# Optimization experiments

Measured on AMD Instinct MI355X. Metric: run time of the kernel, lower is better.

## Reference

```python
import jax, jax.numpy as jnp
import numpy as np


def setup_inputs() -> dict:
    key = jax.random.key(0)
    k1, k2, k3 = jax.random.split(key, 3)
    T, B, C, H, W = 8, 4, 128, 96, 96
    h = w = 384  # original visibility-map resolution
    values = jax.random.normal(k1, (T + 1, B, C, H, W), jnp.float32)
    tvmap = jax.random.uniform(k2, (B, 1, h, w), jnp.float32)
    rvmaps = jax.random.uniform(k3, (T, B, 1, h, w), jnp.float32)
    return {"values": values, "tvmap": tvmap, "rvmaps": rvmaps}


def _resize_bin(m, H, W):
    # bilinear resize (half-pixel centers == torch align_corners=False), then > 0.5 threshold
    r = jax.image.resize(m, m.shape[:-2] + (H, W), method="bilinear")
    return (r > 0.5).astype(m.dtype)


def reference(values, tvmap, rvmaps):
    t_feat = values[0]          # [B,C,H,W]
    r_feats = values[1:]        # [T,B,C,H,W]
    T, B, C, H, W = r_feats.shape

    tv = _resize_bin(tvmap, H, W)                           # [B,1,H,W]
    rv = jax.vmap(lambda m: _resize_bin(m, H, W))(rvmaps)   # [T,B,1,H,W]
    vmap_ = tv[None] * rv                                   # [T,B,1,H,W]

    # per-frame masked similarity score gs
    gs = jnp.sum(vmap_ * t_feat[None] * r_feats, axis=(-1, -2, -3))  # [T,B]
    v_sum = jnp.sum(vmap_[:, :, 0], axis=(-1, -2))                   # [T,B]
    empty = v_sum < 1e-4
    gs = jnp.where(empty, 0.0, gs) / (v_sum + empty.astype(gs.dtype)) / C

    gss = gs.transpose(1, 0)[:, None, :, None, None]   # [B,1,T,1,1]
    vmaps = rv.transpose(1, 2, 0, 3, 4)                # [B,1,T,H,W]

    # masked softmax over frame axis (dim=2) with zero-guard
    mv = gss * vmaps
    mx = jnp.max(mv, axis=2, keepdims=True)
    me = jnp.exp(mv - mx) * vmaps
    ms = jnp.sum(me, axis=2, keepdims=True)
    ms = ms + (ms < 1e-4).astype(ms.dtype)
    c_match = jax.lax.stop_gradient(me / ms)           # [B,1,T,H,W]

    rf = r_feats.transpose(1, 2, 0, 3, 4)              # [B,C,T,H,W]
    c_out = jnp.sum(rf * c_match, axis=2)              # [B,C,H,W]

    c_mask = jnp.sum(c_match * vmaps, axis=2)          # [B,1,H,W]
    c_mask = jax.lax.stop_gradient(1.0 - jnp.mean(c_mask, axis=1, keepdims=True))

    out = jnp.concatenate([t_feat, c_out, c_mask], axis=1)  # [B, 2C+1, H, W]
    return out, c_mask, gs
```

## Files before the change

kernel.cpp:

```cpp
#include <hip/hip_runtime.h>
#include <math.h>

#define T_ 8
#define B_ 4
#define C_ 128
#define HW_ 9216
#define IN_HW_ 147456

__device__ __forceinline__ double resize_px(const float* __restrict__ img, int y, int x) {
  static const double wm[8]  = {0.03125, 0.09375, 0.15625, 0.21875,
                                0.21875, 0.15625, 0.09375, 0.03125};
  static const double w0[8]  = {0.0, 0.0, 0.625/3.5, 0.875/3.5,
                                0.875/3.5, 0.625/3.5, 0.375/3.5, 0.125/3.5};
  static const double w95[8] = {0.125/3.5, 0.375/3.5, 0.625/3.5, 0.875/3.5,
                                0.875/3.5, 0.625/3.5, 0.0, 0.0};
  const double* wy = (y == 0) ? w0 : (y == 95 ? w95 : wm);
  const double* wx = (x == 0) ? w0 : (x == 95 ? w95 : wm);
  double acc = 0.0;
#pragma unroll
  for (int ky = 0; ky < 8; ++ky) {
    double wyv = wy[ky];
    if (wyv == 0.0) continue;
    int jy = 4 * y - 2 + ky;
    const float* row = img + jy * 384;
    double ra = 0.0;
#pragma unroll
    for (int kx = 0; kx < 8; ++kx) {
      double wxv = wx[kx];
      if (wxv == 0.0) continue;
      int jx = 4 * x - 2 + kx;
      ra += wxv * (double)row[jx];
    }
    acc += wyv * ra;
  }
  return acc;
}

__device__ __forceinline__ float block_reduce_sum_256(float v) {
  __shared__ float s[256];
  s[threadIdx.x] = v;
  __syncthreads();
  for (int k = 128; k > 0; k >>= 1) {
    if (threadIdx.x < (unsigned)k) s[threadIdx.x] += s[threadIdx.x + k];
    __syncthreads();
  }
  return s[0];
}

__global__ void k_init(float* __restrict__ v_sum) {
  if (threadIdx.x < T_ * B_) v_sum[threadIdx.x] = 0.f;
}

__global__ void k_tv(const float* __restrict__ tvmap, float* __restrict__ tv) {
  int b = blockIdx.y;
  int p = blockIdx.x * 256 + threadIdx.x;
  const float* img = tvmap + (size_t)b * IN_HW_;
  int y = p / 96, x = p % 96;
  tv[(size_t)b * HW_ + p] = (resize_px(img, y, x) > 0.5) ? 1.0f : 0.0f;
}

__global__ void k_rv(const float* __restrict__ rvmaps, const float* __restrict__ tv,
                     float* __restrict__ rv, float* __restrict__ vm,
                     float* __restrict__ v_sum) {
  int tb = blockIdx.y;
  int b = tb % B_;
  int p = blockIdx.x * 256 + threadIdx.x;
  const float* img = rvmaps + (size_t)tb * IN_HW_;
  int y = p / 96, x = p % 96;
  float rvv = (resize_px(img, y, x) > 0.5) ? 1.0f : 0.0f;
  float vmv = rvv * tv[(size_t)b * HW_ + p];
  rv[(size_t)tb * HW_ + p] = rvv;
  vm[(size_t)tb * HW_ + p] = vmv;
  float s = block_reduce_sum_256(vmv);
  if (threadIdx.x == 0) atomicAdd(&v_sum[tb], s);
}

__global__ __launch_bounds__(256) void k_gs(const float* __restrict__ values,
                                            const float* __restrict__ vm,
                                            float* __restrict__ gs_part) {
  int blk = blockIdx.x;
  int c  = blk % C_;
  int tb = blk / C_;
  int b  = tb % B_;
  const float4* rf  = (const float4*)(values + ((size_t)(B_ + tb) * C_ + c) * HW_);
  const float4* tf  = (const float4*)(values + ((size_t)b * C_ + c) * HW_);
  const float4* vmp = (const float4*)(vm + (size_t)tb * HW_);
  float acc = 0.f;
  for (int i = threadIdx.x; i < HW_ / 4; i += 256) {
    float4 m = vmp[i];
    float4 a = tf[i];
    float4 r = rf[i];
    acc += m.x * a.x * r.x + m.y * a.y * r.y + m.z * a.z * r.z + m.w * a.w * r.w;
  }
  float s = block_reduce_sum_256(acc);
  if (threadIdx.x == 0) gs_part[blk] = s;
}

__global__ void k_gsfin(const float* __restrict__ gs_part, const float* __restrict__ v_sum,
                        float* __restrict__ gs, float* __restrict__ out_gs) {
  int i = threadIdx.x;
  if (i < T_ * B_) {
    float s = 0.f;
    for (int c = 0; c < C_; ++c) s += gs_part[i * C_ + c];
    float vs = v_sum[i];
    bool empty = vs < 1e-4f;
    float g = (empty ? 0.f : s) / (vs + (empty ? 1.f : 0.f)) / (float)C_;
    gs[i] = g;
    out_gs[i] = g;
  }
}

__global__ __launch_bounds__(256) void k_epi(const float* __restrict__ values,
                                             const float* __restrict__ rv,
                                             const float* __restrict__ gs,
                                             float* __restrict__ out,
                                             float* __restrict__ out_cmask) {
  int ctile = blockIdx.x;
  int ptile = blockIdx.y;
  int b     = blockIdx.z;
  __shared__ float gsh[T_];
  if (threadIdx.x < T_) gsh[threadIdx.x] = gs[threadIdx.x * B_ + b];
  __syncthreads();

  int p0 = ptile * 1024 + threadIdx.x * 4;

  float4 rv4[T_];
#pragma unroll
  for (int t = 0; t < T_; ++t)
    rv4[t] = *(const float4*)(rv + ((size_t)(t * B_ + b)) * HW_ + p0);

  float cm[T_][4];
  float cmask[4];
#pragma unroll
  for (int j = 0; j < 4; ++j) {
    float mv[T_];
    float mx = -1e30f;
#pragma unroll
    for (int t = 0; t < T_; ++t) {
      float rvv = ((const float*)&rv4[t])[j];
      mv[t] = gsh[t] * rvv;
      mx = fmaxf(mx, mv[t]);
    }
    float e[T_];
    float ms = 0.f;
#pragma unroll
    for (int t = 0; t < T_; ++t) {
      float rvv = ((const float*)&rv4[t])[j];
      e[t] = expf(mv[t] - mx) * rvv;
      ms += e[t];
    }
    if (ms < 1e-4f) ms += 1.f;
    float inv = 1.f / ms;
    float cs = 0.f;
#pragma unroll
    for (int t = 0; t < T_; ++t) {
      cm[t][j] = e[t] * inv;
      cs += cm[t][j] * ((const float*)&rv4[t])[j];
    }
    cmask[j] = 1.f - cs;
  }

  size_t outb = (size_t)b * 257 * HW_;
#pragma unroll 1
  for (int cc = 0; cc < 8; ++cc) {
    int c = ctile * 8 + cc;
    float4 tf = *(const float4*)(values + ((size_t)b * C_ + c) * HW_ + p0);
    *(float4*)(out + outb + (size_t)c * HW_ + p0) = tf;
    float4 acc = {0.f, 0.f, 0.f, 0.f};
#pragma unroll
    for (int t = 0; t < T_; ++t) {
      const float4 r = *(const float4*)(values +
          ((size_t)((1 + t) * B_ + b) * C_ + c) * HW_ + p0);
      acc.x += cm[t][0] * r.x;
      acc.y += cm[t][1] * r.y;
      acc.z += cm[t][2] * r.z;
      acc.w += cm[t][3] * r.w;
    }
    *(float4*)(out + outb + (size_t)(C_ + c) * HW_ + p0) = acc;
  }
  if (ctile == 0) {
    float4 cmv = {cmask[0], cmask[1], cmask[2], cmask[3]};
    *(float4*)(out + outb + (size_t)256 * HW_ + p0) = cmv;
    *(float4*)(out_cmask + (size_t)b * HW_ + p0) = cmv;
  }
}

extern "C" void kernel_launch(void* const* d_in, const int* in_sizes, int n_in,
                              void* d_out, int out_size, void* d_ws, size_t ws_size,
                              hipStream_t stream) {
  const float* values = (const float*)d_in[0];
  const float* tvmap  = (const float*)d_in[1];
  const float* rvmaps = (const float*)d_in[2];
  float* out = (float*)d_out;

  float* ws      = (float*)d_ws;
  float* tv      = ws;
  float* rv      = tv + (size_t)B_ * HW_;
  float* vm      = rv + (size_t)T_ * B_ * HW_;
  float* gs_part = vm + (size_t)T_ * B_ * HW_;
  float* v_sum   = gs_part + T_ * B_ * C_;
  float* gsar    = v_sum + T_ * B_;

  float* out_cmask = out + (size_t)B_ * 257 * HW_;
  float* out_gs    = out_cmask + (size_t)B_ * HW_;

  hipLaunchKernelGGL(k_init,  dim3(1),                dim3(64),  0, stream, v_sum);
  hipLaunchKernelGGL(k_tv,    dim3(HW_ / 256, B_),    dim3(256), 0, stream, tvmap, tv);
  hipLaunchKernelGGL(k_rv,    dim3(HW_ / 256, T_ * B_), dim3(256), 0, stream, rvmaps, tv, rv, vm, v_sum);
  hipLaunchKernelGGL(k_gs,    dim3(T_ * B_ * C_),     dim3(256), 0, stream, values, vm, gs_part);
  hipLaunchKernelGGL(k_gsfin, dim3(1),                dim3(64),  0, stream, gs_part, v_sum, gsar, out_gs);
  hipLaunchKernelGGL(k_epi,   dim3(16, 9, B_),        dim3(256), 0, stream, values, rv, gsar, out, out_cmask);
}
```

Baseline: 346.0 us.

## Fuse mask kernels, restructure gs reduction, halve epilogue tile, nontemporal stores

```diff
diff --git a/kernel.cpp b/kernel.cpp
--- a/kernel.cpp
+++ b/kernel.cpp
@@ -6,6 +6,9 @@
 #define C_ 128
 #define HW_ 9216
 #define IN_HW_ 147456
+#define NCHUNK 3
+
+typedef float nfloat4 __attribute__((ext_vector_type(4)));
 
 __device__ __forceinline__ double resize_px(const float* __restrict__ img, int y, int x) {
   static const double wm[8]  = {0.03125, 0.09375, 0.15625, 0.21875,
@@ -28,81 +31,86 @@
     for (int kx = 0; kx < 8; ++kx) {
       double wxv = wx[kx];
       if (wxv == 0.0) continue;
-      int jx = 4 * x - 2 + kx;
-      ra += wxv * (double)row[jx];
+      ra += wxv * (double)row[4 * x - 2 + kx];
     }
     acc += wyv * ra;
   }
   return acc;
 }
 
-__device__ __forceinline__ float block_reduce_sum_256(float v) {
+__global__ __launch_bounds__(256) void k_masks(const float* __restrict__ tvmap,
+                                               const float* __restrict__ rvmaps,
+                                               float* __restrict__ rv,
+                                               float* __restrict__ vm,
+                                               float* __restrict__ v_part) {
+  int tb = blockIdx.y;
+  int b = tb % B_;
+  int p = blockIdx.x * 256 + threadIdx.x;
+  int y = p / 96, x = p % 96;
+  float tvv = (resize_px(tvmap + (size_t)b * IN_HW_, y, x) > 0.5) ? 1.0f : 0.0f;
+  float rvv = (resize_px(rvmaps + (size_t)tb * IN_HW_, y, x) > 0.5) ? 1.0f : 0.0f;
+  float vmv = rvv * tvv;
+  rv[(size_t)tb * HW_ + p] = rvv;
+  vm[(size_t)tb * HW_ + p] = vmv;
   __shared__ float s[256];
-  s[threadIdx.x] = v;
+  s[threadIdx.x] = vmv;
   __syncthreads();
   for (int k = 128; k > 0; k >>= 1) {
     if (threadIdx.x < (unsigned)k) s[threadIdx.x] += s[threadIdx.x + k];
     __syncthreads();
   }
-  return s[0];
-}
-
-__global__ void k_init(float* __restrict__ v_sum) {
-  if (threadIdx.x < T_ * B_) v_sum[threadIdx.x] = 0.f;
-}
-
-__global__ void k_tv(const float* __restrict__ tvmap, float* __restrict__ tv) {
-  int b = blockIdx.y;
-  int p = blockIdx.x * 256 + threadIdx.x;
-  const float* img = tvmap + (size_t)b * IN_HW_;
-  int y = p / 96, x = p % 96;
-  tv[(size_t)b * HW_ + p] = (resize_px(img, y, x) > 0.5) ? 1.0f : 0.0f;
-}
-
-__global__ void k_rv(const float* __restrict__ rvmaps, const float* __restrict__ tv,
-                     float* __restrict__ rv, float* __restrict__ vm,
-                     float* __restrict__ v_sum) {
-  int tb = blockIdx.y;
-  int b = tb % B_;
-  int p = blockIdx.x * 256 + threadIdx.x;
-  const float* img = rvmaps + (size_t)tb * IN_HW_;
-  int y = p / 96, x = p % 96;
-  float rvv = (resize_px(img, y, x) > 0.5) ? 1.0f : 0.0f;
-  float vmv = rvv * tv[(size_t)b * HW_ + p];
-  rv[(size_t)tb * HW_ + p] = rvv;
-  vm[(size_t)tb * HW_ + p] = vmv;
-  float s = block_reduce_sum_256(vmv);
-  if (threadIdx.x == 0) atomicAdd(&v_sum[tb], s);
+  if (threadIdx.x == 0) v_part[tb * (HW_ / 256) + blockIdx.x] = s[0];
 }
 
 __global__ __launch_bounds__(256) void k_gs(const float* __restrict__ values,
                                             const float* __restrict__ vm,
                                             float* __restrict__ gs_part) {
-  int blk = blockIdx.x;
-  int c  = blk % C_;
-  int tb = blk / C_;
-  int b  = tb % B_;
-  const float4* rf  = (const float4*)(values + ((size_t)(B_ + tb) * C_ + c) * HW_);
-  const float4* tf  = (const float4*)(values + ((size_t)b * C_ + c) * HW_);
-  const float4* vmp = (const float4*)(vm + (size_t)tb * HW_);
-  float acc = 0.f;
-  for (int i = threadIdx.x; i < HW_ / 4; i += 256) {
-    float4 m = vmp[i];
+  int c     = blockIdx.x;
+  int chunk = blockIdx.y;
+  int b     = blockIdx.z;
+  const float4* tf = (const float4*)(values + ((size_t)b * C_ + c) * HW_);
+  float acc[T_];
+#pragma unroll
+  for (int t = 0; t < T_; ++t) acc[t] = 0.f;
+  int i0 = chunk * (HW_ / 4 / NCHUNK);
+#pragma unroll 1
+  for (int k = 0; k < HW_ / 4 / NCHUNK / 256; ++k) {
+    int i = i0 + k * 256 + threadIdx.x;
     float4 a = tf[i];
-    float4 r = rf[i];
-    acc += m.x * a.x * r.x + m.y * a.y * r.y + m.z * a.z * r.z + m.w * a.w * r.w;
-  }
-  float s = block_reduce_sum_256(acc);
-  if (threadIdx.x == 0) gs_part[blk] = s;
-}
-
-__global__ void k_gsfin(const float* __restrict__ gs_part, const float* __restrict__ v_sum,
+#pragma unroll
+    for (int t = 0; t < T_; ++t) {
+      int tb = t * B_ + b;
+      float4 m = ((const float4*)(vm + (size_t)tb * HW_))[i];
+      float4 r = ((const float4*)(values + ((size_t)(B_ + tb) * C_ + c) * HW_))[i];
+      acc[t] += m.x * a.x * r.x + m.y * a.y * r.y + m.z * a.z * r.z + m.w * a.w * r.w;
+    }
+  }
+  __shared__ float part[4][T_];
+  int lane = threadIdx.x & 63, wid = threadIdx.x >> 6;
+#pragma unroll
+  for (int t = 0; t < T_; ++t) {
+    float v = acc[t];
+    for (int off = 32; off > 0; off >>= 1) v += __shfl_down(v, off);
+    if (lane == 0) part[wid][t] = v;
+  }
+  __syncthreads();
+  if (threadIdx.x < T_) {
+    int t = threadIdx.x;
+    float v = part[0][t] + part[1][t] + part[2][t] + part[3][t];
+    gs_part[(size_t)chunk * (T_ * B_ * C_) + (size_t)(t * B_ + b) * C_ + c] = v;
+  }
+}
+
+__global__ void k_gsfin(const float* __restrict__ gs_part, const float* __restrict__ v_part,
                         float* __restrict__ gs, float* __restrict__ out_gs) {
   int i = threadIdx.x;
   if (i < T_ * B_) {
     float s = 0.f;
-    for (int c = 0; c < C_; ++c) s += gs_part[i * C_ + c];
-    float vs = v_sum[i];
+    for (int ch = 0; ch < NCHUNK; ++ch)
+      for (int c = 0; c < C_; ++c)
+        s += gs_part[(size_t)ch * (T_ * B_ * C_) + i * C_ + c];
+    float vs = 0.f;
+    for (int k = 0; k < HW_ / 256; ++k) vs += v_part[i * (HW_ / 256) + k];
     bool empty = vs < 1e-4f;
     float g = (empty ? 0.f : s) / (vs + (empty ? 1.f : 0.f)) / (float)C_;
     gs[i] = g;
@@ -162,11 +170,12 @@
 
   size_t outb = (size_t)b * 257 * HW_;
 #pragma unroll 1
-  for (int cc = 0; cc < 8; ++cc) {
-    int c = ctile * 8 + cc;
+  for (int cc = 0; cc < 4; ++cc) {
+    int c = ctile * 4 + cc;
     float4 tf = *(const float4*)(values + ((size_t)b * C_ + c) * HW_ + p0);
-    *(float4*)(out + outb + (size_t)c * HW_ + p0) = tf;
-    float4 acc = {0.f, 0.f, 0.f, 0.f};
+    nfloat4 tfn = {tf.x, tf.y, tf.z, tf.w};
+    __builtin_nontemporal_store(tfn, (nfloat4*)(out + outb + (size_t)c * HW_ + p0));
+    nfloat4 acc = {0.f, 0.f, 0.f, 0.f};
 #pragma unroll
     for (int t = 0; t < T_; ++t) {
       const float4 r = *(const float4*)(values +
@@ -176,12 +185,12 @@
       acc.z += cm[t][2] * r.z;
       acc.w += cm[t][3] * r.w;
     }
-    *(float4*)(out + outb + (size_t)(C_ + c) * HW_ + p0) = acc;
+    __builtin_nontemporal_store(acc, (nfloat4*)(out + outb + (size_t)(C_ + c) * HW_ + p0));
   }
   if (ctile == 0) {
-    float4 cmv = {cmask[0], cmask[1], cmask[2], cmask[3]};
-    *(float4*)(out + outb + (size_t)256 * HW_ + p0) = cmv;
-    *(float4*)(out_cmask + (size_t)b * HW_ + p0) = cmv;
+    nfloat4 cmv = {cmask[0], cmask[1], cmask[2], cmask[3]};
+    __builtin_nontemporal_store(cmv, (nfloat4*)(out + outb + (size_t)256 * HW_ + p0));
+    __builtin_nontemporal_store(cmv, (nfloat4*)(out_cmask + (size_t)b * HW_ + p0));
   }
 }
 
@@ -194,20 +203,21 @@
   float* out = (float*)d_out;
 
   float* ws      = (float*)d_ws;
-  float* tv      = ws;
-  float* rv      = tv + (size_t)B_ * HW_;
+  float* rv      = ws;
   float* vm      = rv + (size_t)T_ * B_ * HW_;
   float* gs_part = vm + (size_t)T_ * B_ * HW_;
-  float* v_sum   = gs_part + T_ * B_ * C_;
-  float* gsar    = v_sum + T_ * B_;
+  float* v_part  = gs_part + NCHUNK * T_ * B_ * C_;
+  float* gsar    = v_part + T_ * B_ * (HW_ / 256);
 
   float* out_cmask = out + (size_t)B_ * 257 * HW_;
   float* out_gs    = out_cmask + (size_t)B_ * HW_;
 
-  hipLaunchKernelGGL(k_init,  dim3(1),                dim3(64),  0, stream, v_sum);
-  hipLaunchKernelGGL(k_tv,    dim3(HW_ / 256, B_),    dim3(256), 0, stream, tvmap, tv);
-  hipLaunchKernelGGL(k_rv,    dim3(HW_ / 256, T_ * B_), dim3(256), 0, stream, rvmaps, tv, rv, vm, v_sum);
-  hipLaunchKernelGGL(k_gs,    dim3(T_ * B_ * C_),     dim3(256), 0, stream, values, vm, gs_part);
-  hipLaunchKernelGGL(k_gsfin, dim3(1),                dim3(64),  0, stream, gs_part, v_sum, gsar, out_gs);
-  hipLaunchKernelGGL(k_epi,   dim3(16, 9, B_),        dim3(256), 0, stream, values, rv, gsar, out, out_cmask);
-}
+  hipLaunchKernelGGL(k_masks, dim3(HW_ / 256, T_ * B_), dim3(256), 0, stream,
+                     tvmap, rvmaps, rv, vm, v_part);
+  hipLaunchKernelGGL(k_gs,    dim3(C_, NCHUNK, B_),     dim3(256), 0, stream,
+                     values, vm, gs_part);
+  hipLaunchKernelGGL(k_gsfin, dim3(1),                  dim3(64),  0, stream,
+                     gs_part, v_part, gsar, out_gs);
+  hipLaunchKernelGGL(k_epi,   dim3(32, 9, B_),          dim3(256), 0, stream,
+                     values, rv, gsar, out, out_cmask);
+}
```

Result: slower. 358.7 us (+3.7%).
